# Performance work log

Hardware: AMD Instinct MI355X
Metric: run time of the kernel (lower is better)

## Reference

```python
import jax, jax.numpy as jnp
import numpy as np

S = 2048          # sequence length == max_seq_len
B = 256           # input_bits per token
H = 8             # num voting heads
NPER = 12         # RAM bits per neuron: min(similarity_bits, 12)
NPOS = 11         # relative-position bits: ceil(log2(max_seq_len))
SIM = 2 * B + NPOS  # similarity input bits = [query | key | rel_dist]
THRESH = H // 2   # threshold aggregation cutoff
MAXD = S - 1


def setup_inputs() -> dict:
    key = jax.random.key(0)
    k1, k2, k3 = jax.random.split(key, 3)
    tokens = jax.random.randint(k1, (S, B), 0, 2).astype(jnp.int32)      # bit tokens
    conn = jax.random.randint(k2, (H, NPER), 0, SIM).astype(jnp.int32)   # RAM wiring per head
    table = jax.random.randint(k3, (H, 2 ** NPER), 0, 2).astype(jnp.int32)  # RAM contents (0/1)
    return {"tokens": tokens, "conn": conn, "table": table}


def reference(tokens, conn, table):
    powers = (1 << jnp.arange(NPER)).astype(jnp.int32)            # address bit weights
    q_mask = (conn < B).astype(jnp.int32)
    k_mask = ((conn >= B) & (conn < 2 * B)).astype(jnp.int32)
    p_mask = (conn >= 2 * B).astype(jnp.int32)

    # Address decomposes additively over the three concat regions since wiring is fixed.
    tq = jnp.take(tokens, jnp.clip(conn, 0, B - 1), axis=1)        # [S,H,NPER]
    q_contrib = jnp.sum(tq * (q_mask * powers)[None], axis=-1)     # [S,H]
    tk = jnp.take(tokens, jnp.clip(conn - B, 0, B - 1), axis=1)
    k_contrib = jnp.sum(tk * (k_mask * powers)[None], axis=-1)     # [S,H]

    d = jnp.arange(S)
    rel_bits = ((d[:, None] >> jnp.arange(NPOS)[None, :]) & 1).astype(jnp.int32)  # [S,NPOS]
    tp = jnp.take(rel_bits, jnp.clip(conn - 2 * B, 0, NPOS - 1), axis=1)          # [S,H,NPER]
    p_contrib = jnp.sum(tp * (p_mask * powers)[None], axis=-1)     # [S,H] indexed by distance

    i = jnp.arange(S)
    dist = jnp.clip(i[:, None] - i[None, :], 0, MAXD)              # [S,S]
    addr = q_contrib[:, None, :] + k_contrib[None, :, :] + p_contrib[dist]  # [S,S,H]
    head_bits = table[jnp.arange(H)[None, None, :], addr]          # [S,S,H] RAM lookups

    causal = i[None, :] <= i[:, None]
    votes = jnp.where(causal, head_bits.sum(-1), 0)                # [S,S]

    # threshold aggregation: XOR (per-bit parity) of tokens with vote >= THRESH
    include = (votes >= THRESH).astype(jnp.int32)                  # [S,S]
    parity = jnp.einsum('ij,jb->ib', include, tokens) % 2          # [S,B]
    # fallback: first token achieving the max vote when nothing clears threshold
    fallback = tokens[jnp.argmax(votes, axis=1)]                   # [S,B]
    any_included = include.sum(axis=1, keepdims=True) > 0
    out = jnp.where(any_included, parity, fallback)
    return out.astype(jnp.uint8)
```

## Files before the change

### kernel.cpp

```cpp
#include <hip/hip_runtime.h>
#include <stdint.h>

#define S 2048
#define B 256
#define THRESH 4

typedef unsigned long long u64;
typedef uint32_t u32;


__global__ void prep_kernel(const int* __restrict__ tokens,
                            const int* __restrict__ conn,
                            const int* __restrict__ table,
                            u64* __restrict__ ptok,
                            uint16_t* __restrict__ qc,
                            uint16_t* __restrict__ kc,
                            uint16_t* __restrict__ pc,
                            u32* __restrict__ ptab) {
    const int bi = blockIdx.x, tid = threadIdx.x;

    if (bi >= 256) {
        const int m = (bi - 256) * 256 + tid;
        const int* src = table + m * 32;
        u32 v = 0;
        #pragma unroll
        for (int b = 0; b < 32; ++b) v |= (u32)(src[b] & 1) << b;
        ptab[m] = v;
        return;
    }

    __shared__ u32 s_conn[96];
    __shared__ u64 s_row[8][4];
    const int lane = tid & 63, wave = tid >> 6;

    if (tid < 96) s_conn[tid] = (u32)conn[tid];

    const int r0 = bi * 8;
    #pragma unroll
    for (int r = 0; r < 8; ++r) {
        const int t = tokens[(r0 + r) * B + tid];
        const u64 m = __ballot(t != 0);
        if (lane == 0) { s_row[r][wave] = m; ptok[(r0 + r) * 4 + wave] = m; }
    }
    __syncthreads();

    if (tid < 64) {
        const int r = tid >> 3, h = tid & 7;
        const int i = r0 + r;
        int q = 0, k = 0, p = 0;
        #pragma unroll
        for (int n = 0; n < 12; ++n) {
            const int c = (int)s_conn[h * 12 + n];
            if (c < B) {
                q |= (int)((s_row[r][c >> 6] >> (c & 63)) & 1) << n;
            } else if (c < 2 * B) {
                const int cc = c - B;
                k |= (int)((s_row[r][cc >> 6] >> (cc & 63)) & 1) << n;
            } else {
                p |= ((i >> (c - 2 * B)) & 1) << n;
            }
        }
        qc[i * 8 + h] = (uint16_t)q;
        kc[i * 8 + h] = (uint16_t)k;
        pc[i * 8 + h] = (uint16_t)p;
    }
}

__device__ __forceinline__ int vote8(const u32* s_tab, u64 a0, u64 a1) {
    int v = 0;
    #pragma unroll
    for (int h = 0; h < 4; ++h) {
        { u32 w = (u32)(a0 >> (16 * h + 5)) & 127;
          v += (int)((s_tab[h * 128 + w] >> ((u32)(a0 >> (16 * h)) & 31)) & 1); }
        { u32 w = (u32)(a1 >> (16 * h + 5)) & 127;
          v += (int)((s_tab[(h + 4) * 128 + w] >> ((u32)(a1 >> (16 * h)) & 31)) & 1); }
    }
    return v;
}

__launch_bounds__(256)
__global__ void main_kernel(const u64* __restrict__ ptok,
                            const uint16_t* __restrict__ qc,
                            const uint16_t* __restrict__ kc,
                            const uint16_t* __restrict__ pc,
                            const u32* __restrict__ ptab,
                            int* __restrict__ out) {
    __shared__ u32 s_tab[1024];
    __shared__ u64 s_part[8][256];
    __shared__ u64 s_p2[8][32];
    __shared__ u64 s_fin[8];
    __shared__ u64 s_kred[4];

    const int b   = blockIdx.x;
    const int tid = threadIdx.x;
    const int lane = tid & 63, wave = tid >> 6;

    ((uint4*)s_tab)[tid] = ((const uint4*)ptab)[tid];
    __syncthreads();

    const int rowA = (b == 1023) ? 2047 : 2046 - b;
    const int rowB = (b == 1023) ? 1023 : b;
    const int nA    = rowA + 1;
    const int total = nA + rowB + 1;
    const int niter = total >> 9;

    const ulonglong2 qA = *(const ulonglong2*)(qc + rowA * 8);
    const ulonglong2 qB = *(const ulonglong2*)(qc + rowB * 8);

    u64 ax0=0, ax1=0, ax2=0, ax3=0;
    u64 bx0=0, bx1=0, bx2=0, bx3=0;
    u32 bkA = 2047u, bkB = 2047u;

    for (int it = 0; it < niter; ++it) {
        const int v0 = (it << 9) + tid;
        const int v1 = v0 + 256;

        const bool isA0 = (v0 < nA);
        const bool isA1 = (v1 < nA);
        const int j0 = isA0 ? v0 : v0 - nA;
        const int j1 = isA1 ? v1 : v1 - nA;
        const int d0 = (isA0 ? rowA : rowB) - j0;
        const int d1 = (isA1 ? rowA : rowB) - j1;

        const ulonglong2 kk0 = *(const ulonglong2*)(kc + j0 * 8);
        const ulonglong2 pp0 = *(const ulonglong2*)(pc + d0 * 8);
        const ulonglong2 t00 = *(const ulonglong2*)(ptok + j0 * 4);
        const ulonglong2 t01 = *(const ulonglong2*)(ptok + j0 * 4 + 2);
        const ulonglong2 kk1 = *(const ulonglong2*)(kc + j1 * 8);
        const ulonglong2 pp1 = *(const ulonglong2*)(pc + d1 * 8);
        const ulonglong2 t10 = *(const ulonglong2*)(ptok + j1 * 4);
        const ulonglong2 t11 = *(const ulonglong2*)(ptok + j1 * 4 + 2);

        const int vt0 = vote8(s_tab, (isA0 ? qA.x : qB.x) + kk0.x + pp0.x,
                                     (isA0 ? qA.y : qB.y) + kk0.y + pp0.y);
        const int vt1 = vote8(s_tab, (isA1 ? qA.x : qB.x) + kk1.x + pp1.x,
                                     (isA1 ? qA.y : qB.y) + kk1.y + pp1.y);

        const u32 vk0 = ((u32)(vt0 + 1) << 16) | (u32)(2047 - j0);
        const u32 vk1 = ((u32)(vt1 + 1) << 16) | (u32)(2047 - j1);

        if (isA0) { if (vk0 > bkA) bkA = vk0; } else { if (vk0 > bkB) bkB = vk0; }
        if (isA1) { if (vk1 > bkA) bkA = vk1; } else { if (vk1 > bkB) bkB = vk1; }

        if (vt0 >= THRESH) {
            if (isA0) { ax0 ^= t00.x; ax1 ^= t00.y; ax2 ^= t01.x; ax3 ^= t01.y; }
            else      { bx0 ^= t00.x; bx1 ^= t00.y; bx2 ^= t01.x; bx3 ^= t01.y; }
        }
        if (vt1 >= THRESH) {
            if (isA1) { ax0 ^= t10.x; ax1 ^= t10.y; ax2 ^= t11.x; ax3 ^= t11.y; }
            else      { bx0 ^= t10.x; bx1 ^= t10.y; bx2 ^= t11.x; bx3 ^= t11.y; }
        }
    }

    #pragma unroll
    for (int off = 32; off; off >>= 1) {
        bkA = max(bkA, (u32)__shfl_xor((int)bkA, off));
        bkB = max(bkB, (u32)__shfl_xor((int)bkB, off));
    }

    s_part[0][tid] = ax0; s_part[1][tid] = ax1; s_part[2][tid] = ax2; s_part[3][tid] = ax3;
    s_part[4][tid] = bx0; s_part[5][tid] = bx1; s_part[6][tid] = bx2; s_part[7][tid] = bx3;
    if (lane == 0) s_kred[wave] = ((u64)bkA << 32) | bkB;
    __syncthreads();

    {
        const int w = tid >> 5, c = tid & 31;
        u64 x = s_part[w][c]       ^ s_part[w][c + 32]  ^ s_part[w][c + 64]  ^ s_part[w][c + 96]
              ^ s_part[w][c + 128] ^ s_part[w][c + 160] ^ s_part[w][c + 192] ^ s_part[w][c + 224];
        s_p2[w][c] = x;
    }
    __syncthreads();
    if (tid < 64) {
        const int w = tid >> 3, c = tid & 7;
        u64 x = s_p2[w][c] ^ s_p2[w][c + 8] ^ s_p2[w][c + 16] ^ s_p2[w][c + 24];
        x ^= __shfl_xor(x, 4); x ^= __shfl_xor(x, 2); x ^= __shfl_xor(x, 1);
        if (c == 0) s_fin[w] = x;
    }
    __syncthreads();

    const u32 fkA = max(max((u32)(s_kred[0] >> 32), (u32)(s_kred[1] >> 32)),
                        max((u32)(s_kred[2] >> 32), (u32)(s_kred[3] >> 32)));
    const u32 fkB = max(max((u32)s_kred[0], (u32)s_kred[1]),
                        max((u32)s_kred[2], (u32)s_kred[3]));

    const int widx = tid >> 6, bitb = tid & 63;
    int oA, oB;
    if ((fkA >> 16) > THRESH) {
        oA = (int)((s_fin[widx] >> bitb) & 1);
    } else {
        const int bj = 2047 - (int)(fkA & 0xFFFF);
        oA = (int)((ptok[bj * 4 + widx] >> bitb) & 1);
    }
    if ((fkB >> 16) > THRESH) {
        oB = (int)((s_fin[4 + widx] >> bitb) & 1);
    } else {
        const int bj = 2047 - (int)(fkB & 0xFFFF);
        oB = (int)((ptok[bj * 4 + widx] >> bitb) & 1);
    }
    out[rowA * B + tid] = oA;
    out[rowB * B + tid] = oB;
}

extern "C" void kernel_launch(void* const* d_in, const int* in_sizes, int n_in,
                              void* d_out, int out_size, void* d_ws, size_t ws_size,
                              hipStream_t stream) {
    const int* tokens = (const int*)d_in[0];
    const int* conn   = (const int*)d_in[1];
    const int* table  = (const int*)d_in[2];
    int* outp = (int*)d_out;

    uint8_t* ws = (uint8_t*)d_ws;
    u64*      ptok = (u64*)(ws);
    uint16_t* qcp  = (uint16_t*)(ws + 65536);
    uint16_t* kcp  = (uint16_t*)(ws + 98304);
    uint16_t* pcp  = (uint16_t*)(ws + 131072);
    u32*      ptab = (u32*)(ws + 163840);

    prep_kernel<<<260, 256, 0, stream>>>(tokens, conn, table, ptok, qcp, kcp, pcp, ptab);
    main_kernel<<<S / 2, 256, 0, stream>>>(ptok, qcp, kcp, pcp, ptab, outp);
}
```

Baseline: 19.83 us.

## Assign one row per block, shuffle-reduce partials, and split prep across more blocks

The main kernel now launches one block per output row instead of pairing a short and a long row per block, interleaving rows so blocks of different lengths alternate. The shared-memory XOR tree is replaced with wave shuffles plus a small cross-wave reduction, and token bitmasks are loaded only for included keys. The prep kernel handles 4 rows per block to spread work over more blocks. The trade-off is twice as many blocks with uneven per-block work and a reloaded RAM table per block, in exchange for lighter reductions and more occupancy.

```diff
diff --git a/kernel.cpp b/kernel.cpp
--- a/kernel.cpp
+++ b/kernel.cpp
@@ -19,8 +19,8 @@
                             u32* __restrict__ ptab) {
     const int bi = blockIdx.x, tid = threadIdx.x;
 
-    if (bi >= 256) {
-        const int m = (bi - 256) * 256 + tid;
+    if (bi >= 512) {
+        const int m = (bi - 512) * 256 + tid;
         const int* src = table + m * 32;
         u32 v = 0;
         #pragma unroll
@@ -30,21 +30,21 @@
     }
 
     __shared__ u32 s_conn[96];
-    __shared__ u64 s_row[8][4];
+    __shared__ u64 s_row[4][4];
     const int lane = tid & 63, wave = tid >> 6;
 
     if (tid < 96) s_conn[tid] = (u32)conn[tid];
 
-    const int r0 = bi * 8;
+    const int r0 = bi * 4;
     #pragma unroll
-    for (int r = 0; r < 8; ++r) {
+    for (int r = 0; r < 4; ++r) {
         const int t = tokens[(r0 + r) * B + tid];
         const u64 m = __ballot(t != 0);
         if (lane == 0) { s_row[r][wave] = m; ptok[(r0 + r) * 4 + wave] = m; }
     }
     __syncthreads();
 
-    if (tid < 64) {
+    if (tid < 32) {
         const int r = tid >> 3, h = tid & 7;
         const int i = r0 + r;
         int q = 0, k = 0, p = 0;
@@ -78,7 +78,7 @@
     return v;
 }
 
-__launch_bounds__(256)
+__launch_bounds__(256, 8)
 __global__ void main_kernel(const u64* __restrict__ ptok,
                             const uint16_t* __restrict__ qc,
                             const uint16_t* __restrict__ kc,
@@ -86,10 +86,7 @@
                             const u32* __restrict__ ptab,
                             int* __restrict__ out) {
     __shared__ u32 s_tab[1024];
-    __shared__ u64 s_part[8][256];
-    __shared__ u64 s_p2[8][32];
-    __shared__ u64 s_fin[8];
-    __shared__ u64 s_kred[4];
+    __shared__ u64 s_red[4][5];
 
     const int b   = blockIdx.x;
     const int tid = threadIdx.x;
@@ -98,107 +95,63 @@
     ((uint4*)s_tab)[tid] = ((const uint4*)ptab)[tid];
     __syncthreads();
 
-    const int rowA = (b == 1023) ? 2047 : 2046 - b;
-    const int rowB = (b == 1023) ? 1023 : b;
-    const int nA    = rowA + 1;
-    const int total = nA + rowB + 1;
-    const int niter = total >> 9;
+    const int row = (b & 1) ? (2047 - (b >> 1)) : (b >> 1);
+    const int n   = row + 1;
 
-    const ulonglong2 qA = *(const ulonglong2*)(qc + rowA * 8);
-    const ulonglong2 qB = *(const ulonglong2*)(qc + rowB * 8);
+    const u64 q0 = *(const u64*)(qc + row * 8);
+    const u64 q1 = *(const u64*)(qc + row * 8 + 4);
 
-    u64 ax0=0, ax1=0, ax2=0, ax3=0;
-    u64 bx0=0, bx1=0, bx2=0, bx3=0;
-    u32 bkA = 2047u, bkB = 2047u;
+    u64 x0 = 0, x1 = 0, x2 = 0, x3 = 0;
+    u32 bk = 2047u;
 
+    const int niter = (n + 255) >> 8;
+    #pragma unroll 2
     for (int it = 0; it < niter; ++it) {
-        const int v0 = (it << 9) + tid;
-        const int v1 = v0 + 256;
+        const int v = (it << 8) + tid;
+        const int j = min(v, row);
+        const int d = row - j;
 
-        const bool isA0 = (v0 < nA);
-        const bool isA1 = (v1 < nA);
-        const int j0 = isA0 ? v0 : v0 - nA;
-        const int j1 = isA1 ? v1 : v1 - nA;
-        const int d0 = (isA0 ? rowA : rowB) - j0;
-        const int d1 = (isA1 ? rowA : rowB) - j1;
+        const ulonglong2 kk = *(const ulonglong2*)(kc + j * 8);
+        const ulonglong2 pp = *(const ulonglong2*)(pc + d * 8);
 
-        const ulonglong2 kk0 = *(const ulonglong2*)(kc + j0 * 8);
-        const ulonglong2 pp0 = *(const ulonglong2*)(pc + d0 * 8);
-        const ulonglong2 t00 = *(const ulonglong2*)(ptok + j0 * 4);
-        const ulonglong2 t01 = *(const ulonglong2*)(ptok + j0 * 4 + 2);
-        const ulonglong2 kk1 = *(const ulonglong2*)(kc + j1 * 8);
-        const ulonglong2 pp1 = *(const ulonglong2*)(pc + d1 * 8);
-        const ulonglong2 t10 = *(const ulonglong2*)(ptok + j1 * 4);
-        const ulonglong2 t11 = *(const ulonglong2*)(ptok + j1 * 4 + 2);
+        const int vt = vote8(s_tab, q0 + kk.x + pp.x, q1 + kk.y + pp.y);
 
-        const int vt0 = vote8(s_tab, (isA0 ? qA.x : qB.x) + kk0.x + pp0.x,
-                                     (isA0 ? qA.y : qB.y) + kk0.y + pp0.y);
-        const int vt1 = vote8(s_tab, (isA1 ? qA.x : qB.x) + kk1.x + pp1.x,
-                                     (isA1 ? qA.y : qB.y) + kk1.y + pp1.y);
+        const u32 key = ((u32)(vt + 1) << 16) | (u32)(2047 - j);
+        bk = max(bk, key);
 
-        const u32 vk0 = ((u32)(vt0 + 1) << 16) | (u32)(2047 - j0);
-        const u32 vk1 = ((u32)(vt1 + 1) << 16) | (u32)(2047 - j1);
-
-        if (isA0) { if (vk0 > bkA) bkA = vk0; } else { if (vk0 > bkB) bkB = vk0; }
-        if (isA1) { if (vk1 > bkA) bkA = vk1; } else { if (vk1 > bkB) bkB = vk1; }
-
-        if (vt0 >= THRESH) {
-            if (isA0) { ax0 ^= t00.x; ax1 ^= t00.y; ax2 ^= t01.x; ax3 ^= t01.y; }
-            else      { bx0 ^= t00.x; bx1 ^= t00.y; bx2 ^= t01.x; bx3 ^= t01.y; }
-        }
-        if (vt1 >= THRESH) {
-            if (isA1) { ax0 ^= t10.x; ax1 ^= t10.y; ax2 ^= t11.x; ax3 ^= t11.y; }
-            else      { bx0 ^= t10.x; bx1 ^= t10.y; bx2 ^= t11.x; bx3 ^= t11.y; }
+        if ((v <= row) & (vt >= THRESH)) {
+            const ulonglong2 t0 = *(const ulonglong2*)(ptok + j * 4);
+            const ulonglong2 t1 = *(const ulonglong2*)(ptok + j * 4 + 2);
+            x0 ^= t0.x; x1 ^= t0.y; x2 ^= t1.x; x3 ^= t1.y;
         }
     }
 
     #pragma unroll
     for (int off = 32; off; off >>= 1) {
-        bkA = max(bkA, (u32)__shfl_xor((int)bkA, off));
-        bkB = max(bkB, (u32)__shfl_xor((int)bkB, off));
+        bk = max(bk, (u32)__shfl_xor((int)bk, off));
+        x0 ^= __shfl_xor(x0, off); x1 ^= __shfl_xor(x1, off);
+        x2 ^= __shfl_xor(x2, off); x3 ^= __shfl_xor(x3, off);
     }
-
-    s_part[0][tid] = ax0; s_part[1][tid] = ax1; s_part[2][tid] = ax2; s_part[3][tid] = ax3;
-    s_part[4][tid] = bx0; s_part[5][tid] = bx1; s_part[6][tid] = bx2; s_part[7][tid] = bx3;
-    if (lane == 0) s_kred[wave] = ((u64)bkA << 32) | bkB;
-    __syncthreads();
-
-    {
-        const int w = tid >> 5, c = tid & 31;
-        u64 x = s_part[w][c]       ^ s_part[w][c + 32]  ^ s_part[w][c + 64]  ^ s_part[w][c + 96]
-              ^ s_part[w][c + 128] ^ s_part[w][c + 160] ^ s_part[w][c + 192] ^ s_part[w][c + 224];
-        s_p2[w][c] = x;
-    }
-    __syncthreads();
-    if (tid < 64) {
-        const int w = tid >> 3, c = tid & 7;
-        u64 x = s_p2[w][c] ^ s_p2[w][c + 8] ^ s_p2[w][c + 16] ^ s_p2[w][c + 24];
-        x ^= __shfl_xor(x, 4); x ^= __shfl_xor(x, 2); x ^= __shfl_xor(x, 1);
-        if (c == 0) s_fin[w] = x;
+    if (lane == 0) {
+        s_red[wave][0] = x0; s_red[wave][1] = x1;
+        s_red[wave][2] = x2; s_red[wave][3] = x3;
+        s_red[wave][4] = (u64)bk;
     }
     __syncthreads();
 
-    const u32 fkA = max(max((u32)(s_kred[0] >> 32), (u32)(s_kred[1] >> 32)),
-                        max((u32)(s_kred[2] >> 32), (u32)(s_kred[3] >> 32)));
-    const u32 fkB = max(max((u32)s_kred[0], (u32)s_kred[1]),
-                        max((u32)s_kred[2], (u32)s_kred[3]));
+    const u32 fk = max(max((u32)s_red[0][4], (u32)s_red[1][4]),
+                       max((u32)s_red[2][4], (u32)s_red[3][4]));
+    const int widx = tid >> 6, bitb = tid & 63;
+    const u64 xw = s_red[0][widx] ^ s_red[1][widx] ^ s_red[2][widx] ^ s_red[3][widx];
 
-    const int widx = tid >> 6, bitb = tid & 63;
-    int oA, oB;
-    if ((fkA >> 16) > THRESH) {
-        oA = (int)((s_fin[widx] >> bitb) & 1);
+    int o;
+    if ((fk >> 16) > THRESH) {
+        o = (int)((xw >> bitb) & 1);
     } else {
-        const int bj = 2047 - (int)(fkA & 0xFFFF);
-        oA = (int)((ptok[bj * 4 + widx] >> bitb) & 1);
+        const int bj = 2047 - (int)(fk & 0xFFFF);
+        o = (int)((ptok[bj * 4 + widx] >> bitb) & 1);
     }
-    if ((fkB >> 16) > THRESH) {
-        oB = (int)((s_fin[4 + widx] >> bitb) & 1);
-    } else {
-        const int bj = 2047 - (int)(fkB & 0xFFFF);
-        oB = (int)((ptok[bj * 4 + widx] >> bitb) & 1);
-    }
-    out[rowA * B + tid] = oA;
-    out[rowB * B + tid] = oB;
+    out[row * B + tid] = o;
 }
 
 extern "C" void kernel_launch(void* const* d_in, const int* in_sizes, int n_in,
@@ -216,6 +169,6 @@
     uint16_t* pcp  = (uint16_t*)(ws + 131072);
     u32*      ptab = (u32*)(ws + 163840);
 
-    prep_kernel<<<260, 256, 0, stream>>>(tokens, conn, table, ptok, qcp, kcp, pcp, ptab);
-    main_kernel<<<S / 2, 256, 0, stream>>>(ptok, qcp, kcp, pcp, ptab, outp);
+    prep_kernel<<<516, 256, 0, stream>>>(tokens, conn, table, ptok, qcp, kcp, pcp, ptab);
+    main_kernel<<<S, 256, 0, stream>>>(ptok, qcp, kcp, pcp, ptab, outp);
 }
```

New measurement: 22.80 us. +14.9%, slower.
